# Kernel optimization log

Hardware: AMD Instinct MI355X
Metric: run time of the kernel (lower is better)

## Reference

```python
import jax, jax.numpy as jnp
import numpy as np
from jax import lax

SHIFT_SIZE = 5
PAD = SHIFT_SIZE // 2


def _chunk_shifts(C):
    # torch.chunk(x, 5, dim=1): chunk size = ceil(C/5); shift for chunk i is i - PAD
    csz = -(-C // SHIFT_SIZE)
    return jnp.arange(C) // csz - PAD  # (C,) in [-PAD, PAD]


def _shift_along_h(x, shifts):
    # x: (B,C,H,W). Equivalent of pad+chunk+roll(dim=2)+cat+narrow: per-channel
    # zero-filled shift along H (no wraparound since |shift| <= PAD).
    B, C, H, W = x.shape
    xp = jnp.pad(x, ((0, 0), (0, 0), (PAD, PAD), (0, 0)))
    c_idx = jnp.arange(C)[:, None]              # (C,1)
    h_idx = jnp.arange(H)[None, :] + PAD - shifts[:, None]  # (C,H)
    return xp[:, c_idx, h_idx, :]               # (B,C,H,W)


def _shift_along_w(x, shifts):
    return jnp.swapaxes(_shift_along_h(jnp.swapaxes(x, 2, 3), shifts), 2, 3)


def setup_inputs() -> dict:
    key = jax.random.key(0)
    ks = jax.random.split(key, 7)
    B, H, W, C, hidden = 8, 128, 128, 256, 256
    x = jax.random.normal(ks[0], (B, H * W, C), dtype=jnp.float32)
    w1 = jax.random.normal(ks[1], (hidden, C), dtype=jnp.float32) * 0.02
    b1 = jnp.zeros((hidden,), dtype=jnp.float32)
    fan_out = 3 * 3 * hidden // hidden  # groups = hidden
    dw_w = jax.random.normal(ks[2], (hidden, 1, 3, 3), dtype=jnp.float32) * np.sqrt(2.0 / fan_out)
    dw_b = jnp.zeros((hidden,), dtype=jnp.float32)
    w2 = jax.random.normal(ks[3], (C, hidden), dtype=jnp.float32) * 0.02
    b2 = jnp.zeros((C,), dtype=jnp.float32)
    return {"x": x, "H": H, "W": W, "w1": w1, "b1": b1,
            "dw_w": dw_w, "dw_b": dw_b, "w2": w2, "b2": b2}


def reference(x, H, W, w1, b1, dw_w, dw_b, w2, b2):
    B, N, C = x.shape
    shifts = _chunk_shifts(C)

    # --- shift along H, then fc1 ---
    xn = jnp.reshape(jnp.swapaxes(x, 1, 2), (B, C, H, W))
    x_s = _shift_along_h(xn, shifts)
    x_s = jnp.swapaxes(x_s.reshape(B, C, H * W), 1, 2)   # (B,N,C)
    h = x_s @ w1.T + b1                                  # (B,N,hidden)

    # --- depthwise 3x3 conv ---
    Ch = h.shape[-1]
    himg = jnp.reshape(jnp.swapaxes(h, 1, 2), (B, Ch, H, W))
    himg = lax.conv_general_dilated(
        himg, dw_w, window_strides=(1, 1), padding=((1, 1), (1, 1)),
        feature_group_count=Ch,
        dimension_numbers=("NCHW", "OIHW", "NCHW")) + dw_b[None, :, None, None]
    h = jnp.swapaxes(himg.reshape(B, Ch, H * W), 1, 2)

    h = jax.nn.gelu(h, approximate=False)

    # --- shift along W, then fc2 ---
    hn = jnp.reshape(jnp.swapaxes(h, 1, 2), (B, Ch, H, W))
    h_s = _shift_along_w(hn, _chunk_shifts(Ch))
    h_s = jnp.swapaxes(h_s.reshape(B, Ch, H * W), 1, 2)  # (B,N,hidden)
    out = h_s @ w2.T + b2                                # (B,N,C)
    return out
```

## Files before the change

kernel.cpp:

```cpp
#include <hip/hip_runtime.h>
#include <hip/hip_bf16.h>
#include <math.h>

#define Hc   128
#define Wc   128
#define Cc   256
#define Nc   (Hc * Wc)
#define Bn   8
#define Mtot (Bn * Nc)
#define CSZ  52
#define SPAD 2

typedef unsigned short ushort4v __attribute__((ext_vector_type(4)));
typedef unsigned short ushort8  __attribute__((ext_vector_type(8)));
typedef __bf16         bf16x8   __attribute__((ext_vector_type(8)));
typedef float          f32x4    __attribute__((ext_vector_type(4)));

__device__ __forceinline__ float bf2f(unsigned short u) {
    return __uint_as_float(((unsigned)u) << 16);
}
__device__ __forceinline__ unsigned short f2bf(float f) {
    unsigned u = __float_as_uint(f);
    return (unsigned short)((u + 0x7fffu + ((u >> 16) & 1u)) >> 16);
}
__device__ __forceinline__ unsigned pk2bf(float a, float b) {
    unsigned ua = __float_as_uint(a) + 0x8000u;
    unsigned ub = __float_as_uint(b) + 0x8000u;
    return __builtin_amdgcn_perm(ub, ua, 0x07060302);
}
__device__ __forceinline__ void async16(const void* g, void* l) {
    __builtin_amdgcn_global_load_lds(
        (const __attribute__((address_space(1))) unsigned*)g,
        (__attribute__((address_space(3))) unsigned*)l, 16, 0, 0);
}

__global__ __launch_bounds__(256)
void shiftwprep_kernel(const float* __restrict__ x, unsigned short* __restrict__ xb,
                       const float* __restrict__ w1, const float* __restrict__ w2,
                       const float* __restrict__ dw_w,
                       unsigned short* __restrict__ w1b, unsigned short* __restrict__ w2b,
                       float* __restrict__ dwT)
{
    const int gid0 = blockIdx.x * 256 + threadIdx.x;
    if (blockIdx.x < 64) {
        const int g = gid0;
        {
            float4 a = *(const float4*)(w1 + (size_t)g * 4);
            ushort4v o = { f2bf(a.x), f2bf(a.y), f2bf(a.z), f2bf(a.w) };
            *(ushort4v*)(w1b + (size_t)g * 4) = o;
        }
        {
            float4 a = *(const float4*)(w2 + (size_t)g * 4);
            ushort4v o = { f2bf(a.x), f2bf(a.y), f2bf(a.z), f2bf(a.w) };
            *(ushort4v*)(w2b + (size_t)g * 4) = o;
        }
        if (g < 9 * Cc) dwT[(g % 9) * Cc + g / 9] = dw_w[g];
    }
#pragma unroll
    for (int it = 0; it < 4; ++it) {
        const int gid = gid0 + it * (4096 * 256);
        const int row = gid >> 5;
        const int c   = (gid & 31) * 8;
        const int hh  = (row >> 7) & 127;
        const int s0  = c / CSZ - SPAD;
        const int s1  = (c + 4) / CSZ - SPAD;
        const int h0  = hh - s0, h1r = hh - s1;
        float4 v0 = make_float4(0.f, 0.f, 0.f, 0.f);
        float4 v1 = make_float4(0.f, 0.f, 0.f, 0.f);
        if (h0  >= 0 && h0  < Hc)
            v0 = *(const float4*)(x + ((size_t)row + (size_t)(h0 - hh) * Wc) * Cc + c);
        if (h1r >= 0 && h1r < Hc)
            v1 = *(const float4*)(x + ((size_t)row + (size_t)(h1r - hh) * Wc) * Cc + c + 4);
        uint4 o;
        o.x = pk2bf(v0.x, v0.y); o.y = pk2bf(v0.z, v0.w);
        o.z = pk2bf(v1.x, v1.y); o.w = pk2bf(v1.z, v1.w);
        *(uint4*)(xb + (size_t)row * Cc + c) = o;
    }
}

__global__ __launch_bounds__(256)
void fc1_mfma_kernel(const unsigned short* __restrict__ xb, const unsigned short* __restrict__ w1b,
                     const float* __restrict__ b1, unsigned short* __restrict__ h1)
{
    __shared__ __align__(16) unsigned char smem[34816];
    __bf16* As = (__bf16*)smem;
    __bf16* Bs = (__bf16*)(smem + 16384);
    unsigned short* Cs = (unsigned short*)smem;

    const int tid  = threadIdx.x;
    const int lane = tid & 63;
    const int wave = tid >> 6;
    const int wm = (wave >> 1) * 64, wn = (wave & 1) * 64;

    const int lid = ((blockIdx.x & 7) << 8) | (blockIdx.x >> 3);
    const int bx  = lid >> 1;
    const int j0  = (lid & 1) * 128;
    const size_t m0 = (size_t)bx * 128;
    const int idx0 = tid, idx1 = tid + 256;

    const size_t aro0 = (m0 + (idx0 >> 2)) * Cc + (idx0 & 3) * 8;
    const size_t aro1 = (m0 + (idx1 >> 2)) * Cc + (idx1 & 3) * 8;
    const size_t bro0 = (size_t)(j0 + (idx0 >> 2)) * Cc + (idx0 & 3) * 8;
    const size_t bro1 = (size_t)(j0 + (idx1 >> 2)) * Cc + (idx1 & 3) * 8;

    auto stage = [&](int buf, int t) {
        const int k0 = t * 32;
        __bf16* adst = As + buf * 4096;
        __bf16* bdst = Bs + buf * 4096;
        async16(xb  + aro0 + k0, adst + idx0 * 8);
        async16(xb  + aro1 + k0, adst + idx1 * 8);
        async16(w1b + bro0 + k0, bdst + idx0 * 8);
        async16(w1b + bro1 + k0, bdst + idx1 * 8);
    };

    f32x4 acc[4][4] = {};
    const int kq = (lane >> 4) * 8;
    const int rr = lane & 15;

    stage(0, 0);
    __syncthreads();

    int cur = 0;
    for (int t = 0; t < 8; ++t) {
        const int nxt = cur ^ 1;
        if (t < 7) stage(nxt, t + 1);
        bf16x8 a[4], b[4];
        const __bf16* ap = As + cur * 4096;
        const __bf16* bp = Bs + cur * 4096;
#pragma unroll
        for (int i = 0; i < 4; ++i) {
            a[i] = *(const bf16x8*)(ap + (wm + i * 16 + rr) * 32 + kq);
            b[i] = *(const bf16x8*)(bp + (wn + i * 16 + rr) * 32 + kq);
        }
#pragma unroll
        for (int i = 0; i < 4; ++i)
#pragma unroll
            for (int j = 0; j < 4; ++j)
                acc[i][j] = __builtin_amdgcn_mfma_f32_16x16x32_bf16(a[i], b[j], acc[i][j], 0, 0, 0);
        __syncthreads();
        cur = nxt;
    }

    const int cq = (lane >> 4) * 4;
    const int cc = lane & 15;
    float bv[4];
#pragma unroll
    for (int j = 0; j < 4; ++j) bv[j] = b1[j0 + wn + j * 16 + cc];
#pragma unroll
    for (int i = 0; i < 4; ++i)
#pragma unroll
        for (int j = 0; j < 4; ++j) {
            const int col = wn + j * 16 + cc;
#pragma unroll
            for (int rg = 0; rg < 4; ++rg)
                Cs[(wm + i * 16 + cq + rg) * 136 + col] = f2bf(acc[i][j][rg] + bv[j]);
        }
    __syncthreads();
    {
        const int row = tid >> 1, hf = tid & 1;
        const unsigned short* src = Cs + row * 136 + hf * 64;
        unsigned short* dst = h1 + (m0 + row) * Cc + j0 + hf * 64;
#pragma unroll
        for (int i = 0; i < 8; ++i)
            *(uint4*)(dst + i * 8) = *(const uint4*)(src + i * 8);
    }
}

__global__ __launch_bounds__(256)
void dwconv_gelu_scatter_kernel(const unsigned short* __restrict__ h1,
                                const float* __restrict__ dwT, const float* __restrict__ dw_b,
                                unsigned short* __restrict__ gsh)
{
    const int t   = threadIdx.x;
    const int bh  = blockIdx.x;
    const int bb  = bh >> 7, hh = bh & 127;
    const size_t rowb = (size_t)bb * Nc + (size_t)hh * Wc;

    {
        const int wi = t >> 6;
        const int w  = (wi & 2) ? (wi + 124) : wi;
        const int c8 = (t & 63) * 4;
        uint2 z; z.x = 0u; z.y = 0u;
        *(uint2*)(gsh + (rowb + w) * Cc + c8) = z;
    }
    __syncthreads();

    const int cg  = t & 31;
    const int wq  = t >> 5;
    const int c0  = cg * 8;
    const int s0  = c0 / CSZ - SPAD;
    const int s1  = (c0 + 4) / CSZ - SPAD;

#pragma unroll 1
    for (int qtr = 0; qtr < 4; ++qtr) {
        const int wbase = qtr * 32 + wq * 4 - 1;

        float acc[4][8];
        {
            float4 a0 = *(const float4*)(dw_b + c0);
            float4 a1 = *(const float4*)(dw_b + c0 + 4);
#pragma unroll
            for (int i = 0; i < 4; ++i) {
                acc[i][0] = a0.x; acc[i][1] = a0.y; acc[i][2] = a0.z; acc[i][3] = a0.w;
                acc[i][4] = a1.x; acc[i][5] = a1.y; acc[i][6] = a1.z; acc[i][7] = a1.w;
            }
        }

#pragma unroll
        for (int dy = -1; dy <= 1; ++dy) {
            const int y = hh + dy;
            if (y < 0 || y >= Hc) continue;
            const unsigned short* rp = h1 + ((size_t)bb * Nc + (size_t)y * Wc) * Cc + c0;
            float in[6][8];
#pragma unroll
            for (int dx = 0; dx < 6; ++dx) {
                const int w = wbase + dx;
                ushort8 raw = {0, 0, 0, 0, 0, 0, 0, 0};
                if (w >= 0 && w < Wc) raw = *(const ushort8*)(rp + (size_t)w * Cc);
#pragma unroll
                for (int c = 0; c < 8; ++c) in[dx][c] = bf2f(raw[c]);
            }
            const float* wrow = dwT + (dy + 1) * 3 * Cc + c0;
            float wr[3][8];
#pragma unroll
            for (int tx = 0; tx < 3; ++tx) {
                float4 wa = *(const float4*)(wrow + tx * Cc);
                float4 wb = *(const float4*)(wrow + tx * Cc + 4);
                wr[tx][0] = wa.x; wr[tx][1] = wa.y; wr[tx][2] = wa.z; wr[tx][3] = wa.w;
                wr[tx][4] = wb.x; wr[tx][5] = wb.y; wr[tx][6] = wb.z; wr[tx][7] = wb.w;
            }
#pragma unroll
            for (int i = 0; i < 4; ++i)
#pragma unroll
                for (int tx = 0; tx < 3; ++tx)
#pragma unroll
                    for (int c = 0; c < 8; ++c)
                        acc[i][c] += in[i + tx][c] * wr[tx][c];
        }

#pragma unroll
        for (int i = 0; i < 4; ++i) {
            float g[8];
#pragma unroll
            for (int c = 0; c < 8; ++c) {
                const float v = acc[i][c];
                const float u = v * v;
                const float a = __builtin_fmaf(0.0713548162f, u, 1.5957691216f);
                const float e = __expf(v * a);
                g[c] = v * e * __builtin_amdgcn_rcpf(e + 1.0f);
            }
            uint2 lo, hi;
            lo.x = pk2bf(g[0], g[1]); lo.y = pk2bf(g[2], g[3]);
            hi.x = pk2bf(g[4], g[5]); hi.y = pk2bf(g[6], g[7]);
            const int wo = wbase + 1 + i;
            const int w0 = wo + s0, w1 = wo + s1;
            if ((unsigned)w0 < (unsigned)Wc) *(uint2*)(gsh + (rowb + w0) * Cc + c0)     = lo;
            if ((unsigned)w1 < (unsigned)Wc) *(uint2*)(gsh + (rowb + w1) * Cc + c0 + 4) = hi;
        }
    }
}

__global__ __launch_bounds__(256)
void fc2_mfma_kernel(const unsigned short* __restrict__ A, const unsigned short* __restrict__ w2b,
                     const float* __restrict__ b2, float* __restrict__ out)
{
    __shared__ __align__(16) unsigned char smem[32768];
    __bf16* As = (__bf16*)smem;
    __bf16* Bs = (__bf16*)(smem + 16384);

    const int tid  = threadIdx.x;
    const int lane = tid & 63;
    const int wave = tid >> 6;
    const int wm = (wave >> 1) * 64, wn = (wave & 1) * 64;

    const int lid = ((blockIdx.x & 7) << 8) | (blockIdx.x >> 3);
    const size_t m0 = (size_t)(lid >> 1) * 128;
    const int j0 = (lid & 1) * 128;
    const int idx0 = tid, idx1 = tid + 256;

    const size_t aro0 = (m0 + (idx0 >> 2)) * Cc + (idx0 & 3) * 8;
    const size_t aro1 = (m0 + (idx1 >> 2)) * Cc + (idx1 & 3) * 8;
    const size_t bro0 = (size_t)(j0 + (idx0 >> 2)) * Cc + (idx0 & 3) * 8;
    const size_t bro1 = (size_t)(j0 + (idx1 >> 2)) * Cc + (idx1 & 3) * 8;

    auto stage = [&](int buf, int t) {
        const int k0 = t * 32;
        __bf16* adst = As + buf * 4096;
        __bf16* bdst = Bs + buf * 4096;
        async16(A   + aro0 + k0, adst + idx0 * 8);
        async16(A   + aro1 + k0, adst + idx1 * 8);
        async16(w2b + bro0 + k0, bdst + idx0 * 8);
        async16(w2b + bro1 + k0, bdst + idx1 * 8);
    };

    f32x4 acc[4][4] = {};
    const int kq = (lane >> 4) * 8;
    const int rr = lane & 15;

    stage(0, 0);
    __syncthreads();

    int cur = 0;
    for (int t = 0; t < 8; ++t) {
        const int nxt = cur ^ 1;
        if (t < 7) stage(nxt, t + 1);
        bf16x8 a[4], b[4];
        const __bf16* ap = As + cur * 4096;
        const __bf16* bp = Bs + cur * 4096;
#pragma unroll
        for (int i = 0; i < 4; ++i) {
            a[i] = *(const bf16x8*)(ap + (wm + i * 16 + rr) * 32 + kq);
            b[i] = *(const bf16x8*)(bp + (wn + i * 16 + rr) * 32 + kq);
        }
#pragma unroll
        for (int i = 0; i < 4; ++i)
#pragma unroll
            for (int j = 0; j < 4; ++j)
                acc[i][j] = __builtin_amdgcn_mfma_f32_16x16x32_bf16(a[i], b[j], acc[i][j], 0, 0, 0);
        __syncthreads();
        cur = nxt;
    }

    const int cq = (lane >> 4) * 4;
    const int cc = lane & 15;
    float bv[4];
#pragma unroll
    for (int j = 0; j < 4; ++j) bv[j] = b2[j0 + wn + j * 16 + cc];
#pragma unroll
    for (int i = 0; i < 4; ++i)
#pragma unroll
        for (int j = 0; j < 4; ++j) {
            const int col = j0 + wn + j * 16 + cc;
#pragma unroll
            for (int rg = 0; rg < 4; ++rg)
                out[(m0 + wm + i * 16 + cq + rg) * Cc + col] = acc[i][j][rg] + bv[j];
        }
}

extern "C" void kernel_launch(void* const* d_in, const int* in_sizes, int n_in,
                              void* d_out, int out_size, void* d_ws, size_t ws_size,
                              hipStream_t stream) {
    const float* x    = (const float*)d_in[0];
    const float* w1   = (const float*)d_in[3];
    const float* b1   = (const float*)d_in[4];
    const float* dw_w = (const float*)d_in[5];
    const float* dw_b = (const float*)d_in[6];
    const float* w2   = (const float*)d_in[7];
    const float* b2   = (const float*)d_in[8];
    float* out = (float*)d_out;

    unsigned short* h1  = (unsigned short*)d_ws;
    unsigned short* gsh = h1 + (size_t)Mtot * Cc;
    unsigned short* w1b = gsh + (size_t)Mtot * Cc;
    unsigned short* w2b = w1b + 65536;
    float*          dwT = (float*)(w2b + 65536);

    shiftwprep_kernel<<<dim3(4096), dim3(256), 0, stream>>>(x, gsh, w1, w2, dw_w, w1b, w2b, dwT);
    fc1_mfma_kernel<<<dim3(2 * Mtot / 128), dim3(256), 0, stream>>>(gsh, w1b, b1, h1);
    dwconv_gelu_scatter_kernel<<<dim3(Mtot / 128), dim3(256), 0, stream>>>(h1, dwT, dw_b, gsh);
    fc2_mfma_kernel<<<dim3(2 * Mtot / 128), dim3(256), 0, stream>>>(gsh, w2b, b2, out);
}
```

Measured before the change: 353.1 us.

## Triple-buffer fc1/fc2 GEMM K-loop with partial vmcnt waits

Both MFMA GEMM kernels move from double to triple buffering of the A/B tiles. The K loop is fully unrolled and uses inline s_waitcnt vmcnt(4) plus s_barrier, so two stages of async global-to-LDS loads stay in flight instead of draining all loads at every barrier. This aims to hide global load latency behind MFMA work. It costs more LDS per block (48KB), which may lower occupancy, and it relies on hand-counted vmcnt values being correct.

```diff
diff --git a/kernel.cpp b/kernel.cpp
--- a/kernel.cpp
+++ b/kernel.cpp
@@ -33,6 +33,8 @@
         (const __attribute__((address_space(1))) unsigned*)g,
         (__attribute__((address_space(3))) unsigned*)l, 16, 0, 0);
 }
+
+#define FENCE(vm) asm volatile("s_waitcnt vmcnt(" #vm ") lgkmcnt(0)\n\ts_barrier" ::: "memory")
 
 __global__ __launch_bounds__(256)
 void shiftwprep_kernel(const float* __restrict__ x, unsigned short* __restrict__ xb,
@@ -82,9 +84,8 @@
 void fc1_mfma_kernel(const unsigned short* __restrict__ xb, const unsigned short* __restrict__ w1b,
                      const float* __restrict__ b1, unsigned short* __restrict__ h1)
 {
-    __shared__ __align__(16) unsigned char smem[34816];
-    __bf16* As = (__bf16*)smem;
-    __bf16* Bs = (__bf16*)(smem + 16384);
+    __shared__ __align__(16) unsigned char smem[49152];
+    __bf16* base = (__bf16*)smem;
     unsigned short* Cs = (unsigned short*)smem;
 
     const int tid  = threadIdx.x;
@@ -105,8 +106,8 @@
 
     auto stage = [&](int buf, int t) {
         const int k0 = t * 32;
-        __bf16* adst = As + buf * 4096;
-        __bf16* bdst = Bs + buf * 4096;
+        __bf16* adst = base + buf * 8192;
+        __bf16* bdst = adst + 4096;
         async16(xb  + aro0 + k0, adst + idx0 * 8);
         async16(xb  + aro1 + k0, adst + idx1 * 8);
         async16(w1b + bro0 + k0, bdst + idx0 * 8);
@@ -118,28 +119,37 @@
     const int rr = lane & 15;
 
     stage(0, 0);
-    __syncthreads();
-
-    int cur = 0;
-    for (int t = 0; t < 8; ++t) {
-        const int nxt = cur ^ 1;
-        if (t < 7) stage(nxt, t + 1);
-        bf16x8 a[4], b[4];
-        const __bf16* ap = As + cur * 4096;
-        const __bf16* bp = Bs + cur * 4096;
-#pragma unroll
-        for (int i = 0; i < 4; ++i) {
-            a[i] = *(const bf16x8*)(ap + (wm + i * 16 + rr) * 32 + kq);
-            b[i] = *(const bf16x8*)(bp + (wn + i * 16 + rr) * 32 + kq);
-        }
-#pragma unroll
-        for (int i = 0; i < 4; ++i)
-#pragma unroll
-            for (int j = 0; j < 4; ++j)
-                acc[i][j] = __builtin_amdgcn_mfma_f32_16x16x32_bf16(a[i], b[j], acc[i][j], 0, 0, 0);
-        __syncthreads();
-        cur = nxt;
-    }
+    stage(1, 1);
+    FENCE(4);
+
+#define G1_STEP(T, FN)                                                        \
+    {                                                                          \
+        if constexpr ((T) <= 5) stage(((T) + 2) % 3, (T) + 2);                 \
+        bf16x8 a[4], b[4];                                                     \
+        const __bf16* ap = base + ((T) % 3) * 8192;                            \
+        const __bf16* bp = ap + 4096;                                          \
+        _Pragma("unroll")                                                      \
+        for (int i = 0; i < 4; ++i) {                                          \
+            a[i] = *(const bf16x8*)(ap + (wm + i * 16 + rr) * 32 + kq);        \
+            b[i] = *(const bf16x8*)(bp + (wn + i * 16 + rr) * 32 + kq);        \
+        }                                                                      \
+        _Pragma("unroll")                                                      \
+        for (int i = 0; i < 4; ++i)                                            \
+            _Pragma("unroll")                                                  \
+            for (int j = 0; j < 4; ++j)                                        \
+                acc[i][j] = __builtin_amdgcn_mfma_f32_16x16x32_bf16(a[i], b[j], acc[i][j], 0, 0, 0); \
+        FN;                                                                    \
+    }
+
+    G1_STEP(0, FENCE(4));
+    G1_STEP(1, FENCE(4));
+    G1_STEP(2, FENCE(4));
+    G1_STEP(3, FENCE(4));
+    G1_STEP(4, FENCE(4));
+    G1_STEP(5, FENCE(4));
+    G1_STEP(6, FENCE(0));
+    G1_STEP(7, __syncthreads());
+#undef G1_STEP
 
     const int cq = (lane >> 4) * 4;
     const int cc = lane & 15;
@@ -264,9 +274,8 @@
 void fc2_mfma_kernel(const unsigned short* __restrict__ A, const unsigned short* __restrict__ w2b,
                      const float* __restrict__ b2, float* __restrict__ out)
 {
-    __shared__ __align__(16) unsigned char smem[32768];
-    __bf16* As = (__bf16*)smem;
-    __bf16* Bs = (__bf16*)(smem + 16384);
+    __shared__ __align__(16) unsigned char smem[49152];
+    __bf16* base = (__bf16*)smem;
 
     const int tid  = threadIdx.x;
     const int lane = tid & 63;
@@ -285,8 +294,8 @@
 
     auto stage = [&](int buf, int t) {
         const int k0 = t * 32;
-        __bf16* adst = As + buf * 4096;
-        __bf16* bdst = Bs + buf * 4096;
+        __bf16* adst = base + buf * 8192;
+        __bf16* bdst = adst + 4096;
         async16(A   + aro0 + k0, adst + idx0 * 8);
         async16(A   + aro1 + k0, adst + idx1 * 8);
         async16(w2b + bro0 + k0, bdst + idx0 * 8);
@@ -298,28 +307,37 @@
     const int rr = lane & 15;
 
     stage(0, 0);
-    __syncthreads();
-
-    int cur = 0;
-    for (int t = 0; t < 8; ++t) {
-        const int nxt = cur ^ 1;
-        if (t < 7) stage(nxt, t + 1);
-        bf16x8 a[4], b[4];
-        const __bf16* ap = As + cur * 4096;
-        const __bf16* bp = Bs + cur * 4096;
-#pragma unroll
-        for (int i = 0; i < 4; ++i) {
-            a[i] = *(const bf16x8*)(ap + (wm + i * 16 + rr) * 32 + kq);
-            b[i] = *(const bf16x8*)(bp + (wn + i * 16 + rr) * 32 + kq);
-        }
-#pragma unroll
-        for (int i = 0; i < 4; ++i)
-#pragma unroll
-            for (int j = 0; j < 4; ++j)
-                acc[i][j] = __builtin_amdgcn_mfma_f32_16x16x32_bf16(a[i], b[j], acc[i][j], 0, 0, 0);
-        __syncthreads();
-        cur = nxt;
-    }
+    stage(1, 1);
+    FENCE(4);
+
+#define G2_STEP(T, FN)                                                        \
+    {                                                                          \
+        if constexpr ((T) <= 5) stage(((T) + 2) % 3, (T) + 2);                 \
+        bf16x8 a[4], b[4];                                                     \
+        const __bf16* ap = base + ((T) % 3) * 8192;                            \
+        const __bf16* bp = ap + 4096;                                          \
+        _Pragma("unroll")                                                      \
+        for (int i = 0; i < 4; ++i) {                                          \
+            a[i] = *(const bf16x8*)(ap + (wm + i * 16 + rr) * 32 + kq);        \
+            b[i] = *(const bf16x8*)(bp + (wn + i * 16 + rr) * 32 + kq);        \
+        }                                                                      \
+        _Pragma("unroll")                                                      \
+        for (int i = 0; i < 4; ++i)                                            \
+            _Pragma("unroll")                                                  \
+            for (int j = 0; j < 4; ++j)                                        \
+                acc[i][j] = __builtin_amdgcn_mfma_f32_16x16x32_bf16(a[i], b[j], acc[i][j], 0, 0, 0); \
+        FN;                                                                    \
+    }
+
+    G2_STEP(0, FENCE(4));
+    G2_STEP(1, FENCE(4));
+    G2_STEP(2, FENCE(4));
+    G2_STEP(3, FENCE(4));
+    G2_STEP(4, FENCE(4));
+    G2_STEP(5, FENCE(4));
+    G2_STEP(6, FENCE(0));
+    G2_STEP(7, ;);
+#undef G2_STEP
 
     const int cq = (lane >> 4) * 4;
     const int cc = lane & 15;
```

New measurement: 350.2 us (median of 2 runs). No clear change (-0.8%).
